# Kernel tuning notes

Measured on AMD Instinct MI355X. Metric: run time of the kernel, lower is better.

Reference implementation:

```python
import jax, jax.numpy as jnp
import numpy as np

D_MODEL = 1024
H = 16
D_K = D_MODEL // H
B, S = 4, 2048


def setup_inputs() -> dict:
    key = jax.random.key(0)
    ks = jax.random.split(key, 12)
    s = 1.0 / np.sqrt(D_MODEL)
    inp = {
        "q": jax.random.normal(ks[0], (B, S, D_MODEL), jnp.float32),
        "k": jax.random.normal(ks[1], (B, S, D_MODEL), jnp.float32),
        "v": jax.random.normal(ks[2], (B, S, D_MODEL), jnp.float32),
        "mask": jax.random.randint(ks[3], (1, 1, S, S), 0, 2, jnp.int32),
        # torch nn.Linear convention: weight [out, in], y = x @ W.T + b
        "w_q": jax.random.uniform(ks[4], (D_MODEL, D_MODEL), jnp.float32, -s, s),
        "b_q": jax.random.uniform(ks[5], (D_MODEL,), jnp.float32, -s, s),
        "w_k": jax.random.uniform(ks[6], (D_MODEL, D_MODEL), jnp.float32, -s, s),
        "b_k": jax.random.uniform(ks[7], (D_MODEL,), jnp.float32, -s, s),
        "w_v": jax.random.uniform(ks[8], (D_MODEL, D_MODEL), jnp.float32, -s, s),
        "b_v": jax.random.uniform(ks[9], (D_MODEL,), jnp.float32, -s, s),
        "w_o": jax.random.uniform(ks[10], (D_MODEL, D_MODEL), jnp.float32, -s, s),
        "b_o": jax.random.uniform(ks[11], (D_MODEL,), jnp.float32, -s, s),
    }
    return inp


def _split_heads(x):
    b, s, _ = x.shape
    return x.reshape(b, s, H, D_K).transpose(0, 2, 1, 3)  # [B,H,S,Dk]


def reference(q, k, v, mask, w_q, b_q, w_k, b_k, w_v, b_v, w_o, b_o):
    query = _split_heads(q @ w_q.T + b_q)
    key = _split_heads(k @ w_k.T + b_k)
    value = _split_heads(v @ w_v.T + b_v)
    scores = jnp.einsum("bhqd,bhkd->bhqk", query, key) / jnp.sqrt(
        jnp.asarray(D_K, query.dtype))
    scores = jnp.where(mask == 0, jnp.asarray(-1e9, scores.dtype), scores)
    attn = jax.nn.softmax(scores, axis=-1)  # dropout p=0 (eval) -> identity
    x = jnp.einsum("bhqk,bhkd->bhqd", attn, value)
    x = x.transpose(0, 2, 1, 3).reshape(q.shape[0], -1, H * D_K)
    return x @ w_o.T + b_o
```

## Files before the change

kernel.cpp:

```cpp
#include <hip/hip_runtime.h>

typedef __bf16 bf16_t;
typedef __bf16 bf16x4 __attribute__((ext_vector_type(4)));
typedef __bf16 bf16x8 __attribute__((ext_vector_type(8)));
typedef float f32x4 __attribute__((ext_vector_type(4)));
typedef float f32x16 __attribute__((ext_vector_type(16)));
typedef unsigned int uint;
typedef uint uint2v __attribute__((ext_vector_type(2)));
typedef uint uint4v __attribute__((ext_vector_type(4)));

#define CSCALE 0.18033688011112042f

static __device__ __forceinline__ bf16_t f2bf(float f) {
  unsigned u = __builtin_bit_cast(unsigned, f);
  u = (u + 0x7fff + ((u >> 16) & 1)) >> 16;
  unsigned short h = (unsigned short)u;
  return __builtin_bit_cast(bf16_t, h);
}
static __device__ __forceinline__ uint cvt_pk(float a, float b) {
  uint r;
  asm("v_cvt_pk_bf16_f32 %0, %1, %2" : "=v"(r) : "v"(a), "v"(b));
  return r;
}

#define GLD_LDS(g, l) \
  __builtin_amdgcn_global_load_lds((const __attribute__((address_space(1))) void*)(g), \
                                   (__attribute__((address_space(3))) void*)(l), 16, 0, 0)
#define VMCNT(n) asm volatile("s_waitcnt vmcnt(" #n ")" ::: "memory")
#define LGKM0() asm volatile("s_waitcnt lgkmcnt(0)" ::: "memory")
#define BARRIER() do { __builtin_amdgcn_s_barrier(); __builtin_amdgcn_sched_barrier(0); } while (0)

__global__ void cvt4_f2b(const float* __restrict__ a, const float* __restrict__ b,
                         const float* __restrict__ c, const float* __restrict__ d,
                         bf16_t* __restrict__ oa, bf16_t* __restrict__ ob,
                         bf16_t* __restrict__ oc, bf16_t* __restrict__ od) {
  int i = blockIdx.x * 256 + threadIdx.x;
  const float* src = a;
  bf16_t* dst = oa;
  int w = i >> 18;
  i &= 262143;
  if (w == 1) { src = b; dst = ob; }
  else if (w == 2) { src = c; dst = oc; }
  else if (w == 3) { src = d; dst = od; }
  const float4 f = reinterpret_cast<const float4*>(src)[i];
  bf16x4 o;
  o[0] = f2bf(f.x); o[1] = f2bf(f.y); o[2] = f2bf(f.z); o[3] = f2bf(f.w);
  reinterpret_cast<bf16x4*>(dst)[i] = o;
}

__global__ void mask_bits_k(const int* __restrict__ m, uint* __restrict__ out) {
  int i = blockIdx.x * 256 + threadIdx.x;
  int q = i & 2047, t = i >> 11;
  const int* mrow = m + (size_t)q * 2048 + t * 32;
  uint bits = 0;
#pragma unroll
  for (int j = 0; j < 16; ++j) {
    int r0 = (j & 3) + 8 * (j >> 2);
    bits |= (mrow[r0] ? 1u : 0u) << j;
    bits |= (mrow[r0 + 4] ? 1u : 0u) << (16 + j);
  }
  out[(size_t)t * 2048 + q] = bits;
}

__global__ __launch_bounds__(256, 2) void qkv_gemm(
    const float* __restrict__ qA, const float* __restrict__ kA, const float* __restrict__ vA,
    const bf16_t* __restrict__ wq, const bf16_t* __restrict__ wk, const bf16_t* __restrict__ wv,
    const float* __restrict__ bq, const float* __restrict__ bk, const float* __restrict__ bv,
    bf16_t* __restrict__ Qp, bf16_t* __restrict__ Kp, bf16_t* __restrict__ Vt) {
  constexpr int K = 1024;
  __shared__ __align__(16) bf16_t AsB[2][128 * 32];
  __shared__ __align__(16) bf16_t BsB[3][256 * 32];
  const int z = blockIdx.z;
  const float* A = (z == 0) ? qA : (z == 1) ? kA : vA;
  const bf16_t* W = (z == 0) ? wq : (z == 1) ? wk : wv;
  const float* bias = (z == 0) ? bq : (z == 1) ? bk : bv;

  const int tid = threadIdx.x;
  const int lane = tid & 63;
  const int wv_ = tid >> 6;
  const int wm = (wv_ & 1) * 64, wn = (wv_ >> 1) * 128;
  const int l15 = lane & 15, lhi = lane >> 4;
  const int bm = blockIdx.x, bn = blockIdx.y;

  const int arow0 = tid >> 3;
  const int acol = tid & 7;
  const float* gA = A + (size_t)(bm * 128 + arow0) * K + acol * 4;
  const int brows = tid >> 2;
  const bf16_t* gB = W + (size_t)(bn * 256 + brows) * K + ((tid & 3) ^ (brows & 3)) * 8;

  f32x4 acc[4][8] = {};
  f32x4 rA0[4], rA1[4];

  auto A_LOAD = [&](int t, f32x4* R) {
#pragma unroll
    for (int L = 0; L < 4; ++L)
      R[L] = *reinterpret_cast<const f32x4*>(gA + (size_t)L * 32 * K + t * 32);
  };
  auto A_WRITE = [&](const f32x4* R, int buf) {
#pragma unroll
    for (int L = 0; L < 4; ++L) {
      int row = arow0 + L * 32;
      uint2v u;
      u[0] = cvt_pk(R[L][0], R[L][1]);
      u[1] = cvt_pk(R[L][2], R[L][3]);
      char* p = (char*)&AsB[buf][0] + row * 64 + (((acol >> 1) ^ (row & 3)) * 16) + (acol & 1) * 8;
      *reinterpret_cast<uint2v*>(p) = u;
    }
  };
  auto B_STAGE = [&](int t, int buf) {
#pragma unroll
    for (int c2 = 0; c2 < 4; ++c2)
      GLD_LDS(gB + (size_t)c2 * 64 * K + t * 32, (char*)&BsB[buf][0] + c2 * 4096 + wv_ * 1024);
  };
  auto COMPUTE = [&](int ba, int bb) {
    bf16x8 af[4], bfv[8];
#pragma unroll
    for (int i = 0; i < 4; ++i) {
      int arow = wm + i * 16 + l15;
      af[i] = *reinterpret_cast<const bf16x8*>(
          (const char*)&AsB[ba][0] + arow * 64 + ((lhi ^ (arow & 3)) * 16));
    }
#pragma unroll
    for (int j = 0; j < 8; ++j) {
      int br = wn + j * 16 + l15;
      bfv[j] = *reinterpret_cast<const bf16x8*>(
          (const char*)&BsB[bb][0] + br * 64 + ((lhi ^ (br & 3)) * 16));
    }
#pragma unroll
    for (int i = 0; i < 4; ++i)
#pragma unroll
      for (int j = 0; j < 8; ++j)
        acc[i][j] = __builtin_amdgcn_mfma_f32_16x16x32_bf16(af[i], bfv[j], acc[i][j], 0, 0, 0);
  };

#define QSTEP(T, RL, RW, BAW, BAC, BBC, BBS) \
  A_LOAD((T) + 2, RL); B_STAGE((T) + 2, BBS); \
  COMPUTE(BAC, BBC); \
  VMCNT(8); \
  A_WRITE(RW, BAW); \
  LGKM0(); BARRIER();

  A_LOAD(0, rA0); B_STAGE(0, 0);
  A_LOAD(1, rA1); B_STAGE(1, 1);
  VMCNT(8);
  A_WRITE(rA0, 0);
  LGKM0(); BARRIER();

#pragma unroll 1
  for (int t6 = 0; t6 < 30; t6 += 6) {
    QSTEP(t6 + 0, rA0, rA1, 1, 0, 0, 2)
    QSTEP(t6 + 1, rA1, rA0, 0, 1, 1, 0)
    QSTEP(t6 + 2, rA0, rA1, 1, 0, 2, 1)
    QSTEP(t6 + 3, rA1, rA0, 0, 1, 0, 2)
    QSTEP(t6 + 4, rA0, rA1, 1, 0, 1, 0)
    QSTEP(t6 + 5, rA1, rA0, 0, 1, 2, 1)
  }
  COMPUTE(0, 0);
  VMCNT(4);
  A_WRITE(rA1, 1);
  VMCNT(0);
  LGKM0(); BARRIER();
  COMPUTE(1, 1);

  if (z == 2) {
    const int b = (bm * 128) >> 11;
    const int s0 = (bm * 128) & 2047;
    bf16_t* vb = Vt + ((size_t)b * 1024 + bn * 256 + wn + l15) * 2048 + s0 + wm + lhi * 4;
#pragma unroll
    for (int j = 0; j < 8; ++j) {
      float bv2 = bias[bn * 256 + wn + j * 16 + l15];
#pragma unroll
      for (int i = 0; i < 4; ++i) {
        bf16x4 pk;
#pragma unroll
        for (int r = 0; r < 4; ++r) pk[r] = f2bf(acc[i][j][r] + bv2);
        *reinterpret_cast<bf16x4*>(vb + (size_t)(j * 16) * 2048 + i * 16) = pk;
      }
    }
  } else {
    bf16_t* O = (z == 0) ? Qp : Kp;
    const float scale = (z == 0) ? CSCALE : 1.0f;
#pragma unroll
    for (int i = 0; i < 4; ++i) {
#pragma unroll
      for (int j = 0; j < 8; ++j) {
        int n = bn * 256 + wn + j * 16 + l15;
        float bv2 = bias[n];
#pragma unroll
        for (int r = 0; r < 4; ++r) {
          int m = bm * 128 + wm + i * 16 + lhi * 4 + r;
          O[(size_t)m * 1024 + n] = f2bf((acc[i][j][r] + bv2) * scale);
        }
      }
    }
  }
#undef QSTEP
}

__global__ __launch_bounds__(256, 2) void gemm_o(
    const bf16_t* __restrict__ A, const bf16_t* __restrict__ Bw,
    const float* __restrict__ bias, float* __restrict__ Cout) {
  constexpr int K = 1024;
  __shared__ __align__(16) bf16_t As[3][128 * 32];
  __shared__ __align__(16) bf16_t Bs[3][256 * 32];
  const int tid = threadIdx.x;
  const int lane = tid & 63;
  const int wv_ = tid >> 6;
  const int wm = (wv_ & 1) * 64, wn = (wv_ >> 1) * 128;
  const int l15 = lane & 15, lhi = lane >> 4;
  const int bm = blockIdx.x, bn = blockIdx.y;
  const int rws = tid >> 2;
  const bf16_t* ga = A + (size_t)(bm * 128 + rws) * K + ((tid & 3) ^ (rws & 3)) * 8;
  const bf16_t* gb = Bw + (size_t)(bn * 256 + rws) * K + ((tid & 3) ^ (rws & 3)) * 8;
  f32x4 acc[4][8] = {};

  auto STAGE = [&](int t, int buf) {
#pragma unroll
    for (int c2 = 0; c2 < 2; ++c2)
      GLD_LDS(ga + (size_t)c2 * 64 * K + t * 32, (char*)&As[buf][0] + c2 * 4096 + wv_ * 1024);
#pragma unroll
    for (int c2 = 0; c2 < 4; ++c2)
      GLD_LDS(gb + (size_t)c2 * 64 * K + t * 32, (char*)&Bs[buf][0] + c2 * 4096 + wv_ * 1024);
  };
  auto COMPUTE = [&](int buf) {
    bf16x8 af[4], bfv[8];
#pragma unroll
    for (int i = 0; i < 4; ++i) {
      int arow = wm + i * 16 + l15;
      af[i] = *reinterpret_cast<const bf16x8*>(
          (const char*)&As[buf][0] + arow * 64 + ((lhi ^ (arow & 3)) * 16));
    }
#pragma unroll
    for (int j = 0; j < 8; ++j) {
      int br = wn + j * 16 + l15;
      bfv[j] = *reinterpret_cast<const bf16x8*>(
          (const char*)&Bs[buf][0] + br * 64 + ((lhi ^ (br & 3)) * 16));
    }
#pragma unroll
    for (int i = 0; i < 4; ++i)
#pragma unroll
      for (int j = 0; j < 8; ++j)
        acc[i][j] = __builtin_amdgcn_mfma_f32_16x16x32_bf16(af[i], bfv[j], acc[i][j], 0, 0, 0);
  };

  STAGE(0, 0);
  STAGE(1, 1);
#pragma unroll 1
  for (int tt = 0; tt < 30; tt += 3) {
    VMCNT(6); BARRIER(); COMPUTE(0); STAGE(tt + 2, 2);
    VMCNT(6); BARRIER(); COMPUTE(1); STAGE(tt + 3, 0);
    VMCNT(6); BARRIER(); COMPUTE(2); STAGE(tt + 4, 1);
  }
  VMCNT(6); BARRIER(); COMPUTE(0);
  VMCNT(0); BARRIER(); COMPUTE(1);

#pragma unroll
  for (int i = 0; i < 4; ++i)
#pragma unroll
    for (int j = 0; j < 8; ++j) {
      int n = bn * 256 + wn + j * 16 + l15;
      float bv2 = bias[n];
#pragma unroll
      for (int r = 0; r < 4; ++r) {
        int m = bm * 128 + wm + i * 16 + lhi * 4 + r;
        Cout[(size_t)m * 1024 + n] = acc[i][j][r] + bv2;
      }
    }
}

static __device__ __forceinline__ f32x16 qk_tile(const bf16_t* Kbuf, const bf16x8 qf[4],
                                                 int l31, int h) {
  f32x16 s = {};
  __builtin_amdgcn_s_setprio(1);
#pragma unroll
  for (int c = 0; c < 4; ++c) {
    bf16x8 kf = *reinterpret_cast<const bf16x8*>(Kbuf + l31 * 72 + h * 8 + 16 * c);
    s = __builtin_amdgcn_mfma_f32_32x32x16_bf16(kf, qf[c], s, 0, 0, 0);
  }
  __builtin_amdgcn_s_setprio(0);
  return s;
}

static __device__ __forceinline__ void softmax_tile(
    const f32x16& sv, uint mb, int h, f32x16& o0, f32x16& o1,
    float& mrun, float& lsum, bf16x8& pa0, bf16x8& pa1) {
  const uint mbh = mb >> (h << 4);
  float a0 = fmaxf(fmaxf(sv[0], sv[1]), sv[2]);
  float a1 = fmaxf(fmaxf(sv[3], sv[4]), sv[5]);
  float a2 = fmaxf(fmaxf(sv[6], sv[7]), sv[8]);
  float a3 = fmaxf(fmaxf(sv[9], sv[10]), sv[11]);
  float a4 = fmaxf(fmaxf(sv[12], sv[13]), sv[14]);
  float b0 = fmaxf(fmaxf(a0, a1), a2);
  float mt = fmaxf(fmaxf(b0, fmaxf(a3, a4)), sv[15]);
  if (!__all(mt - mrun <= 8.0f)) {
    float mtf = fmaxf(mt, __shfl_xor(mt, 32));
    float mnew = fmaxf(mrun, mtf);
    float alpha = __builtin_amdgcn_exp2f(mrun - mnew);
    lsum *= alpha;
#pragma unroll
    for (int r = 0; r < 16; ++r) {
      float ar = __shfl(alpha, (r & 3) + 8 * (r >> 2) + 4 * h);
      o0[r] *= ar; o1[r] *= ar;
    }
    mrun = mnew;
  }
  float p[16];
#pragma unroll
  for (int r = 0; r < 16; ++r) {
    float pv = __builtin_amdgcn_exp2f(sv[r] - mrun);
    uint smask = (uint)__builtin_amdgcn_sbfe((int)mbh, r, 1);
    p[r] = __builtin_bit_cast(float, __builtin_bit_cast(uint, pv) & smask);
  }
  float t0 = p[0] + p[1], t1 = p[2] + p[3], t2 = p[4] + p[5], t3 = p[6] + p[7];
  float t4 = p[8] + p[9], t5 = p[10] + p[11], t6 = p[12] + p[13], t7 = p[14] + p[15];
  t0 += t1; t2 += t3; t4 += t5; t6 += t7;
  lsum += (t0 + t2) + (t4 + t6);
  uint dw[8];
#pragma unroll
  for (int i = 0; i < 8; ++i) dw[i] = cvt_pk(p[2 * i], p[2 * i + 1]);
  uint e0 = (uint)__shfl_xor((int)(h ? dw[0] : dw[2]), 32);
  uint e1 = (uint)__shfl_xor((int)(h ? dw[1] : dw[3]), 32);
  uint e2 = (uint)__shfl_xor((int)(h ? dw[4] : dw[6]), 32);
  uint e3 = (uint)__shfl_xor((int)(h ? dw[5] : dw[7]), 32);
  uint4v ua0 = {h ? e0 : dw[0], h ? e1 : dw[1], h ? dw[2] : e0, h ? dw[3] : e1};
  uint4v ua1 = {h ? e2 : dw[4], h ? e3 : dw[5], h ? dw[6] : e2, h ? dw[7] : e3};
  pa0 = __builtin_bit_cast(bf16x8, ua0);
  pa1 = __builtin_bit_cast(bf16x8, ua1);
}

static __device__ __forceinline__ void pv_tile(const bf16_t* Vbuf, bf16x8 pa0, bf16x8 pa1,
                                               int l31, int h, f32x16& o0, f32x16& o1) {
  bf16x8 v00 = *reinterpret_cast<const bf16x8*>(Vbuf + l31 * 40 + h * 8);
  bf16x8 v01 = *reinterpret_cast<const bf16x8*>(Vbuf + l31 * 40 + 16 + h * 8);
  bf16x8 v10 = *reinterpret_cast<const bf16x8*>(Vbuf + (32 + l31) * 40 + h * 8);
  bf16x8 v11 = *reinterpret_cast<const bf16x8*>(Vbuf + (32 + l31) * 40 + 16 + h * 8);
  __builtin_amdgcn_s_setprio(1);
  o0 = __builtin_amdgcn_mfma_f32_32x32x16_bf16(pa0, v00, o0, 0, 0, 0);
  o0 = __builtin_amdgcn_mfma_f32_32x32x16_bf16(pa1, v01, o0, 0, 0, 0);
  o1 = __builtin_amdgcn_mfma_f32_32x32x16_bf16(pa0, v10, o1, 0, 0, 0);
  o1 = __builtin_amdgcn_mfma_f32_32x32x16_bf16(pa1, v11, o1, 0, 0, 0);
  __builtin_amdgcn_s_setprio(0);
}

__global__ __launch_bounds__(256, 4) void attn_kernel(
    const bf16_t* __restrict__ Qp, const bf16_t* __restrict__ Kp,
    const bf16_t* __restrict__ Vt, const uint* __restrict__ maskbits,
    bf16_t* __restrict__ Xb) {
  constexpr int S = 2048, D = 1024;
  __shared__ __align__(16) bf16_t Ks[2][32][72];
  __shared__ __align__(16) bf16_t Vs[2][64][40];
  const int tid = threadIdx.x;
  const int wv_ = tid >> 6, lane = tid & 63;
  const int l31 = lane & 31, h = lane >> 5;
  const int blk = blockIdx.x;
  const int bh = blk & 63, qt4 = blk >> 6;
  const int b = bh >> 4, hd = bh & 15;
  const int q0 = qt4 * 128 + wv_ * 32;

  const int rK = tid >> 3, sK = tid & 7;
  const int rV = tid >> 2, sV = tid & 3;
  const bf16_t* gK = Kp + ((size_t)b * S + rK) * D + hd * 64 + sK * 8;
  const bf16_t* gV = Vt + ((size_t)b * 1024 + hd * 64 + rV) * (size_t)S + sV * 8;
  bf16_t* wK0 = &Ks[0][rK][sK * 8];
  bf16_t* wK1 = &Ks[1][rK][sK * 8];
  bf16_t* wV0 = &Vs[0][rV][sV * 8];
  bf16_t* wV1 = &Vs[1][rV][sV * 8];

  const bf16_t* qbase = Qp + (size_t)(b * S + q0 + l31) * D + hd * 64 + h * 8;
  bf16x8 qf[4];
#pragma unroll
  for (int c = 0; c < 4; ++c)
    qf[c] = *reinterpret_cast<const bf16x8*>(qbase + 16 * c);

  const uint* mbase = maskbits + q0 + l31;

  f32x16 o0 = {}, o1 = {};
  float mrun = 0.f, lsum = 0.f;
  bf16x8 pa0, pa1;

  {
    bf16x8 k0 = *reinterpret_cast<const bf16x8*>(gK);
    bf16x8 k1 = *reinterpret_cast<const bf16x8*>(gK + (size_t)32 * D);
    bf16x8 v0 = *reinterpret_cast<const bf16x8*>(gV);
    *reinterpret_cast<bf16x8*>(wK0) = k0;
    *reinterpret_cast<bf16x8*>(wK1) = k1;
    *reinterpret_cast<bf16x8*>(wV0) = v0;
  }
  uint mb0 = mbase[0];
  __syncthreads();
  {
    f32x16 s = qk_tile(&Ks[0][0][0], qf, l31, h);
    softmax_tile(s, mb0, h, o0, o1, mrun, lsum, pa0, pa1);
  }

  auto body = [&](int j, bf16_t* wK_st, bf16_t* wV_st, const bf16_t* Kq,
                  const bf16_t* Vp, bool stageK) {
    bf16x8 kreg, vreg;
    if (stageK) kreg = *reinterpret_cast<const bf16x8*>(gK + (size_t)(j + 2) * 32 * D);
    vreg = *reinterpret_cast<const bf16x8*>(gV + (size_t)(j + 1) * 32);
    uint mbn = mbase[(size_t)(j + 1) * 2048];
    f32x16 s = qk_tile(Kq, qf, l31, h);
    pv_tile(Vp, pa0, pa1, l31, h, o0, o1);
    softmax_tile(s, mbn, h, o0, o1, mrun, lsum, pa0, pa1);
    if (stageK) *reinterpret_cast<bf16x8*>(wK_st) = kreg;
    *reinterpret_cast<bf16x8*>(wV_st) = vreg;
    __syncthreads();
  };

#pragma unroll 1
  for (int jj = 0; jj < 31; ++jj) {
    const int j = 2 * jj;
    body(j,     wK0, wV1, &Ks[1][0][0], &Vs[0][0][0], true);
    body(j + 1, wK1, wV0, &Ks[0][0][0], &Vs[1][0][0], true);
  }
  body(62, wK0, wV1, &Ks[1][0][0], &Vs[0][0][0], false);
  pv_tile(&Vs[1][0][0], pa0, pa1, l31, h, o0, o1);

  lsum += __shfl_xor(lsum, 32);
  float linv = __builtin_amdgcn_rcpf(lsum);
  bf16_t* xrow = Xb + (size_t)(b * S + q0) * D + hd * 64 + l31;
#pragma unroll
  for (int r = 0; r < 16; ++r) {
    int qrow = (r & 3) + 8 * (r >> 2) + 4 * h;
    float lr = __shfl(linv, qrow);
    xrow[(size_t)qrow * D] = f2bf(o0[r] * lr);
    xrow[(size_t)qrow * D + 32] = f2bf(o1[r] * lr);
  }
}

extern "C" void kernel_launch(void* const* d_in, const int* in_sizes, int n_in,
                              void* d_out, int out_size, void* d_ws, size_t ws_size,
                              hipStream_t stream) {
  const float* q = (const float*)d_in[0];
  const float* k = (const float*)d_in[1];
  const float* v = (const float*)d_in[2];
  const int* mask = (const int*)d_in[3];
  const float* w_q = (const float*)d_in[4];
  const float* b_q = (const float*)d_in[5];
  const float* w_k = (const float*)d_in[6];
  const float* b_k = (const float*)d_in[7];
  const float* w_v = (const float*)d_in[8];
  const float* b_v = (const float*)d_in[9];
  const float* w_o = (const float*)d_in[10];
  const float* b_o = (const float*)d_in[11];

  char* ws = (char*)d_ws;
  const size_t SZ = (size_t)8192 * 1024 * 2;
  bf16_t* Qp = (bf16_t*)(ws + 0 * SZ);
  bf16_t* Kp = (bf16_t*)(ws + 1 * SZ);
  bf16_t* Vt = (bf16_t*)(ws + 2 * SZ);
  bf16_t* Xb = (bf16_t*)(ws + 3 * SZ);
  uint* maskB = (uint*)(ws + 4 * SZ);
  bf16_t* wqb = (bf16_t*)(ws + 4 * SZ + 8388608);
  bf16_t* wkb = wqb + 1048576;
  bf16_t* wvb = wkb + 1048576;
  bf16_t* wob = wvb + 1048576;

  cvt4_f2b<<<4096, 256, 0, stream>>>(w_q, w_k, w_v, w_o, wqb, wkb, wvb, wob);
  mask_bits_k<<<512, 256, 0, stream>>>(mask, maskB);

  dim3 g3(64, 4, 3);
  qkv_gemm<<<g3, 256, 0, stream>>>(q, k, v, wqb, wkb, wvb, b_q, b_k, b_v, Qp, Kp, Vt);
  attn_kernel<<<1024, 256, 0, stream>>>(Qp, Kp, Vt, maskB, Xb);
  gemm_o<<<dim3(64, 4), 256, 0, stream>>>(Xb, wob, b_o, (float*)d_out);
}
```

Measured before the change: 237.9 us.

## Process two 32-row query tiles per wave to reuse K/V LDS fragments

```diff
diff --git a/kernel.cpp b/kernel.cpp
--- a/kernel.cpp
+++ b/kernel.cpp
@@ -268,17 +268,18 @@
     }
 }
 
-static __device__ __forceinline__ f32x16 qk_tile(const bf16_t* Kbuf, const bf16x8 qf[4],
-                                                 int l31, int h) {
-  f32x16 s = {};
+static __device__ __forceinline__ void qk2(const bf16_t* Kbuf, const bf16x8 qfA[4],
+                                           const bf16x8 qfB[4], int l31, int h,
+                                           f32x16& sA, f32x16& sB) {
+  sA = {}; sB = {};
   __builtin_amdgcn_s_setprio(1);
 #pragma unroll
   for (int c = 0; c < 4; ++c) {
     bf16x8 kf = *reinterpret_cast<const bf16x8*>(Kbuf + l31 * 72 + h * 8 + 16 * c);
-    s = __builtin_amdgcn_mfma_f32_32x32x16_bf16(kf, qf[c], s, 0, 0, 0);
+    sA = __builtin_amdgcn_mfma_f32_32x32x16_bf16(kf, qfA[c], sA, 0, 0, 0);
+    sB = __builtin_amdgcn_mfma_f32_32x32x16_bf16(kf, qfB[c], sB, 0, 0, 0);
   }
   __builtin_amdgcn_s_setprio(0);
-  return s;
 }
 
 static __device__ __forceinline__ void softmax_tile(
@@ -328,21 +329,27 @@
   pa1 = __builtin_bit_cast(bf16x8, ua1);
 }
 
-static __device__ __forceinline__ void pv_tile(const bf16_t* Vbuf, bf16x8 pa0, bf16x8 pa1,
-                                               int l31, int h, f32x16& o0, f32x16& o1) {
+static __device__ __forceinline__ void pv2(const bf16_t* Vbuf,
+                                           bf16x8 paA0, bf16x8 paA1, bf16x8 paB0, bf16x8 paB1,
+                                           int l31, int h,
+                                           f32x16& oA0, f32x16& oA1, f32x16& oB0, f32x16& oB1) {
   bf16x8 v00 = *reinterpret_cast<const bf16x8*>(Vbuf + l31 * 40 + h * 8);
   bf16x8 v01 = *reinterpret_cast<const bf16x8*>(Vbuf + l31 * 40 + 16 + h * 8);
   bf16x8 v10 = *reinterpret_cast<const bf16x8*>(Vbuf + (32 + l31) * 40 + h * 8);
   bf16x8 v11 = *reinterpret_cast<const bf16x8*>(Vbuf + (32 + l31) * 40 + 16 + h * 8);
   __builtin_amdgcn_s_setprio(1);
-  o0 = __builtin_amdgcn_mfma_f32_32x32x16_bf16(pa0, v00, o0, 0, 0, 0);
-  o0 = __builtin_amdgcn_mfma_f32_32x32x16_bf16(pa1, v01, o0, 0, 0, 0);
-  o1 = __builtin_amdgcn_mfma_f32_32x32x16_bf16(pa0, v10, o1, 0, 0, 0);
-  o1 = __builtin_amdgcn_mfma_f32_32x32x16_bf16(pa1, v11, o1, 0, 0, 0);
+  oA0 = __builtin_amdgcn_mfma_f32_32x32x16_bf16(paA0, v00, oA0, 0, 0, 0);
+  oA0 = __builtin_amdgcn_mfma_f32_32x32x16_bf16(paA1, v01, oA0, 0, 0, 0);
+  oA1 = __builtin_amdgcn_mfma_f32_32x32x16_bf16(paA0, v10, oA1, 0, 0, 0);
+  oA1 = __builtin_amdgcn_mfma_f32_32x32x16_bf16(paA1, v11, oA1, 0, 0, 0);
+  oB0 = __builtin_amdgcn_mfma_f32_32x32x16_bf16(paB0, v00, oB0, 0, 0, 0);
+  oB0 = __builtin_amdgcn_mfma_f32_32x32x16_bf16(paB1, v01, oB0, 0, 0, 0);
+  oB1 = __builtin_amdgcn_mfma_f32_32x32x16_bf16(paB0, v10, oB1, 0, 0, 0);
+  oB1 = __builtin_amdgcn_mfma_f32_32x32x16_bf16(paB1, v11, oB1, 0, 0, 0);
   __builtin_amdgcn_s_setprio(0);
 }
 
-__global__ __launch_bounds__(256, 4) void attn_kernel(
+__global__ __launch_bounds__(256, 2) void attn_kernel(
     const bf16_t* __restrict__ Qp, const bf16_t* __restrict__ Kp,
     const bf16_t* __restrict__ Vt, const uint* __restrict__ maskbits,
     bf16_t* __restrict__ Xb) {
@@ -353,9 +360,9 @@
   const int wv_ = tid >> 6, lane = tid & 63;
   const int l31 = lane & 31, h = lane >> 5;
   const int blk = blockIdx.x;
-  const int bh = blk & 63, qt4 = blk >> 6;
+  const int bh = blk & 63, qt = blk >> 6;
   const int b = bh >> 4, hd = bh & 15;
-  const int q0 = qt4 * 128 + wv_ * 32;
+  const int q0 = qt * 256 + wv_ * 64;
 
   const int rK = tid >> 3, sK = tid & 7;
   const int rV = tid >> 2, sV = tid & 3;
@@ -367,16 +374,18 @@
   bf16_t* wV1 = &Vs[1][rV][sV * 8];
 
   const bf16_t* qbase = Qp + (size_t)(b * S + q0 + l31) * D + hd * 64 + h * 8;
-  bf16x8 qf[4];
-#pragma unroll
-  for (int c = 0; c < 4; ++c)
-    qf[c] = *reinterpret_cast<const bf16x8*>(qbase + 16 * c);
+  bf16x8 qfA[4], qfB[4];
+#pragma unroll
+  for (int c = 0; c < 4; ++c) {
+    qfA[c] = *reinterpret_cast<const bf16x8*>(qbase + 16 * c);
+    qfB[c] = *reinterpret_cast<const bf16x8*>(qbase + (size_t)32 * D + 16 * c);
+  }
 
   const uint* mbase = maskbits + q0 + l31;
 
-  f32x16 o0 = {}, o1 = {};
-  float mrun = 0.f, lsum = 0.f;
-  bf16x8 pa0, pa1;
+  f32x16 oA0 = {}, oA1 = {}, oB0 = {}, oB1 = {};
+  float mrunA = 0.f, lsumA = 0.f, mrunB = 0.f, lsumB = 0.f;
+  bf16x8 paA0, paA1, paB0, paB1;
 
   {
     bf16x8 k0 = *reinterpret_cast<const bf16x8*>(gK);
@@ -386,11 +395,13 @@
     *reinterpret_cast<bf16x8*>(wK1) = k1;
     *reinterpret_cast<bf16x8*>(wV0) = v0;
   }
-  uint mb0 = mbase[0];
+  uint mbA = mbase[0], mbB = mbase[32];
   __syncthreads();
   {
-    f32x16 s = qk_tile(&Ks[0][0][0], qf, l31, h);
-    softmax_tile(s, mb0, h, o0, o1, mrun, lsum, pa0, pa1);
+    f32x16 sA, sB;
+    qk2(&Ks[0][0][0], qfA, qfB, l31, h, sA, sB);
+    softmax_tile(sA, mbA, h, oA0, oA1, mrunA, lsumA, paA0, paA1);
+    softmax_tile(sB, mbB, h, oB0, oB1, mrunB, lsumB, paB0, paB1);
   }
 
   auto body = [&](int j, bf16_t* wK_st, bf16_t* wV_st, const bf16_t* Kq,
@@ -398,10 +409,13 @@
     bf16x8 kreg, vreg;
     if (stageK) kreg = *reinterpret_cast<const bf16x8*>(gK + (size_t)(j + 2) * 32 * D);
     vreg = *reinterpret_cast<const bf16x8*>(gV + (size_t)(j + 1) * 32);
-    uint mbn = mbase[(size_t)(j + 1) * 2048];
-    f32x16 s = qk_tile(Kq, qf, l31, h);
-    pv_tile(Vp, pa0, pa1, l31, h, o0, o1);
-    softmax_tile(s, mbn, h, o0, o1, mrun, lsum, pa0, pa1);
+    uint mnA = mbase[(size_t)(j + 1) * 2048];
+    uint mnB = mbase[(size_t)(j + 1) * 2048 + 32];
+    f32x16 sA, sB;
+    qk2(Kq, qfA, qfB, l31, h, sA, sB);
+    pv2(Vp, paA0, paA1, paB0, paB1, l31, h, oA0, oA1, oB0, oB1);
+    softmax_tile(sA, mnA, h, oA0, oA1, mrunA, lsumA, paA0, paA1);
+    softmax_tile(sB, mnB, h, oB0, oB1, mrunB, lsumB, paB0, paB1);
     if (stageK) *reinterpret_cast<bf16x8*>(wK_st) = kreg;
     *reinterpret_cast<bf16x8*>(wV_st) = vreg;
     __syncthreads();
@@ -414,17 +428,22 @@
     body(j + 1, wK1, wV0, &Ks[0][0][0], &Vs[1][0][0], true);
   }
   body(62, wK0, wV1, &Ks[1][0][0], &Vs[0][0][0], false);
-  pv_tile(&Vs[1][0][0], pa0, pa1, l31, h, o0, o1);
-
-  lsum += __shfl_xor(lsum, 32);
-  float linv = __builtin_amdgcn_rcpf(lsum);
+  pv2(&Vs[1][0][0], paA0, paA1, paB0, paB1, l31, h, oA0, oA1, oB0, oB1);
+
+  lsumA += __shfl_xor(lsumA, 32);
+  lsumB += __shfl_xor(lsumB, 32);
+  float linvA = __builtin_amdgcn_rcpf(lsumA);
+  float linvB = __builtin_amdgcn_rcpf(lsumB);
   bf16_t* xrow = Xb + (size_t)(b * S + q0) * D + hd * 64 + l31;
 #pragma unroll
   for (int r = 0; r < 16; ++r) {
     int qrow = (r & 3) + 8 * (r >> 2) + 4 * h;
-    float lr = __shfl(linv, qrow);
-    xrow[(size_t)qrow * D] = f2bf(o0[r] * lr);
-    xrow[(size_t)qrow * D + 32] = f2bf(o1[r] * lr);
+    float lrA = __shfl(linvA, qrow);
+    float lrB = __shfl(linvB, qrow);
+    xrow[(size_t)qrow * D] = f2bf(oA0[r] * lrA);
+    xrow[(size_t)qrow * D + 32] = f2bf(oA1[r] * lrA);
+    xrow[(size_t)(qrow + 32) * D] = f2bf(oB0[r] * lrB);
+    xrow[(size_t)(qrow + 32) * D + 32] = f2bf(oB1[r] * lrB);
   }
 }
 
@@ -461,6 +480,6 @@
 
   dim3 g3(64, 4, 3);
   qkv_gemm<<<g3, 256, 0, stream>>>(q, k, v, wqb, wkb, wvb, b_q, b_k, b_v, Qp, Kp, Vt);
-  attn_kernel<<<1024, 256, 0, stream>>>(Qp, Kp, Vt, maskB, Xb);
+  attn_kernel<<<512, 256, 0, stream>>>(Qp, Kp, Vt, maskB, Xb);
   gemm_o<<<dim3(64, 4), 256, 0, stream>>>(Xb, wob, b_o, (float*)d_out);
 }
```

Result: no change. 235.1 us (-1.2%).
